# Kernel tuning notes

Measured on AMD Instinct MI355X. Metric: run time of the kernel, lower is better.

## Reference

```python
import jax, jax.numpy as jnp
import numpy as np

EPS = 1e-5

def conv3x3(x, w, b, stride=1):
    y = jax.lax.conv_general_dilated(x, w, (stride, stride), 'SAME',
                                     dimension_numbers=('NCHW', 'OIHW', 'NCHW'))
    return y + b[None, :, None, None]

def batchnorm_train(x, gamma, beta):
    # training-mode BN: batch statistics over (N, H, W)
    mean = x.mean(axis=(0, 2, 3), keepdims=True)
    var = x.var(axis=(0, 2, 3), keepdims=True)
    xh = (x - mean) * jax.lax.rsqrt(var + EPS)
    return xh * gamma[None, :, None, None] + beta[None, :, None, None]

def haar_dwt2(x):
    # pywt.dwt2(x, 'db1') on last two axes; even H,W so 'symmetric' padding is a no-op.
    # a = (x0 + x1)/sqrt2, d = (x0 - x1)/sqrt2 per axis -> 2x2 block combinations / 2.
    x00 = x[:, :, 0::2, 0::2]
    x01 = x[:, :, 0::2, 1::2]
    x10 = x[:, :, 1::2, 0::2]
    x11 = x[:, :, 1::2, 1::2]
    cA = (x00 + x01 + x10 + x11) * 0.5
    cH = (x00 + x01 - x10 - x11) * 0.5  # pywt 'da': detail along rows
    cV = (x00 - x01 + x10 - x11) * 0.5  # pywt 'ad': detail along cols
    cD = (x00 - x01 - x10 + x11) * 0.5
    return cA, cH, cV, cD


def setup_inputs() -> dict:
    key = jax.random.key(0)
    ks = jax.random.split(key, 8)
    N, in_c, out_c, H, W = 4, 3, 64, 512, 512

    def kaiming(k, shape):
        fan_in = shape[1] * shape[2] * shape[3]
        return jax.random.normal(k, shape, jnp.float32) * np.sqrt(2.0 / fan_in)

    inputs = jax.random.normal(ks[0], (N, in_c, H, W), jnp.float32)
    return {
        'inputs': inputs,
        # conv_block: conv1 -> bn1 -> conv2 -> bn2 -> relu
        'w1': kaiming(ks[1], (out_c, in_c, 3, 3)),
        'b1': jnp.zeros((out_c,), jnp.float32),
        'g1': jnp.ones((out_c,), jnp.float32),
        'be1': jnp.zeros((out_c,), jnp.float32),
        'w2': kaiming(ks[2], (out_c, out_c, 3, 3)),
        'b2': jnp.zeros((out_c,), jnp.float32),
        'g2': jnp.ones((out_c,), jnp.float32),
        'be2': jnp.zeros((out_c,), jnp.float32),
        # conv_dwt_block: conv(out_c*4 -> out_c) -> bn -> relu
        'w3': kaiming(ks[3], (out_c, out_c * 4, 3, 3)),
        'b3': jnp.zeros((out_c,), jnp.float32),
        'g3': jnp.ones((out_c,), jnp.float32),
        'be3': jnp.zeros((out_c,), jnp.float32),
    }


def reference(inputs, w1, b1, g1, be1, w2, b2, g2, be2, w3, b3, g3, be3):
    # conv_block
    x = conv3x3(inputs, w1, b1)
    x = batchnorm_train(x, g1, be1)
    x = conv3x3(x, w2, b2)
    x = batchnorm_train(x, g2, be2)
    skip_con = jax.nn.relu(x)

    # original detaches skip_con before the (CPU pywt) DWT -> no grad through this branch
    dwt_in = jax.lax.stop_gradient(skip_con)
    cA, cH, cV, cD = haar_dwt2(dwt_in)
    dwt = jnp.concatenate((cA, cH, cV, cD), axis=1)  # [N, 4*out_c, H/2, W/2]

    y = conv3x3(dwt, w3, b3)
    y = batchnorm_train(y, g3, be3)
    dwt_out = jax.nn.relu(y)
    return dwt_out, skip_con
```

## Files before the change

### kernel.cpp

```cpp
#include <hip/hip_runtime.h>
#include <cstdint>

typedef float f32x4 __attribute__((ext_vector_type(4)));
typedef __bf16 bf16x8 __attribute__((ext_vector_type(8)));
typedef unsigned int uint32;
typedef unsigned short ushort_t;

__device__ __forceinline__ ushort_t f2bf(float f) {
    uint32 u = __builtin_bit_cast(uint32, f);
    u = (u + 0x7fffu + ((u >> 16) & 1u)) >> 16;
    return (ushort_t)u;
}
__device__ __forceinline__ float bf2f(ushort_t h) {
    return __builtin_bit_cast(float, (uint32)h << 16);
}

__global__ __launch_bounds__(256) void im2col1_kernel(
    const float* __restrict__ in,
    ushort_t* __restrict__ P)
{
    int px = blockIdx.x * 256 + threadIdx.x;
    int n = px >> 18, rem = px & 262143;
    int y = rem >> 9, x = rem & 511;
    ushort_t pv[32];
#pragma unroll
    for (int ci = 0; ci < 3; ++ci)
#pragma unroll
        for (int t = 0; t < 9; ++t) {
            int dy = t / 3 - 1, dx = t % 3 - 1;
            int yy = y + dy, xx = x + dx;
            bool v = ((unsigned)yy < 512u) && ((unsigned)xx < 512u);
            pv[ci * 9 + t] = v ? f2bf(in[((n * 3 + ci) * 512 + yy) * 512 + xx])
                               : (ushort_t)0;
        }
#pragma unroll
    for (int k = 27; k < 32; ++k) pv[k] = 0;
    uint4* dst = (uint4*)(P + (size_t)px * 32);
    dst[0] = *(uint4*)(pv);
    dst[1] = *(uint4*)(pv + 8);
    dst[2] = *(uint4*)(pv + 16);
    dst[3] = *(uint4*)(pv + 24);
}

__global__ void prepw1_kernel(const float* __restrict__ w1,
                              ushort_t* __restrict__ Wsw1)
{
    int i = blockIdx.x * 256 + threadIdx.x;
    int ii = i & 7, lane = (i >> 3) & 63, nt = i >> 9;
    int cout = nt * 16 + (lane & 15);
    int k = (lane >> 4) * 8 + ii;
    Wsw1[i] = (k < 27) ? f2bf(w1[cout * 27 + k]) : (ushort_t)0;
}

__global__ __launch_bounds__(256) void gemm1_kernel(
    const ushort_t* __restrict__ P,
    const ushort_t* __restrict__ Wsw1,
    const float* __restrict__ b1,
    ushort_t* __restrict__ X1)
{
    int tid = threadIdx.x;
    int wave = tid >> 6, lane = tid & 63;
    int lp = lane & 15, lg = lane >> 4;
    int pxb = blockIdx.x * 256 + wave * 64;

    bf16x8 wf[4];
#pragma unroll
    for (int nt = 0; nt < 4; ++nt)
        wf[nt] = *(const bf16x8*)(Wsw1 + (nt * 64 + lane) * 8);

    f32x4 acc[4][4];
#pragma unroll
    for (int a = 0; a < 4; ++a)
#pragma unroll
        for (int b = 0; b < 4; ++b) acc[a][b] = (f32x4){0.f, 0.f, 0.f, 0.f};

#pragma unroll
    for (int nf = 0; nf < 4; ++nf) {
        bf16x8 bfrag = *(const bf16x8*)(P + (size_t)(pxb + nf * 16 + lp) * 32 + lg * 8);
#pragma unroll
        for (int nt = 0; nt < 4; ++nt)
            acc[nt][nf] = __builtin_amdgcn_mfma_f32_16x16x32_bf16(
                wf[nt], bfrag, acc[nt][nf], 0, 0, 0);
    }

#pragma unroll
    for (int nf = 0; nf < 4; ++nf) {
        size_t px = (size_t)pxb + nf * 16 + lp;
#pragma unroll
        for (int nt = 0; nt < 4; ++nt) {
            ushort_t ov[4];
#pragma unroll
            for (int r = 0; r < 4; ++r)
                ov[r] = f2bf(acc[nt][nf][r] + b1[nt * 16 + lg * 4 + r]);
            *(ushort4*)(X1 + px * 64 + nt * 16 + lg * 4) = *(ushort4*)ov;
        }
    }
}

__global__ __launch_bounds__(256) void stats_kernel(
    const ushort_t* __restrict__ X, float* __restrict__ sums, int Mpx)
{
    int tid = threadIdx.x;
    int cb = (tid & 7) * 8;
    int pr = tid >> 3;
    float s[8], q[8];
#pragma unroll
    for (int j = 0; j < 8; ++j) { s[j] = 0.f; q[j] = 0.f; }

    for (int p = blockIdx.x * 32 + pr; p < Mpx; p += gridDim.x * 32) {
        uint4 raw = *(const uint4*)(X + (size_t)p * 64 + cb);
        const ushort_t* up = (const ushort_t*)&raw;
#pragma unroll
        for (int j = 0; j < 8; ++j) {
            float f = bf2f(up[j]);
            s[j] += f; q[j] += f * f;
        }
    }
    __shared__ float ls[32][64];
#pragma unroll
    for (int j = 0; j < 8; ++j) ls[pr][cb + j] = s[j];
    __syncthreads();
    float S = 0.f;
    if (tid < 64) for (int r = 0; r < 32; ++r) S += ls[r][tid];
    __syncthreads();
#pragma unroll
    for (int j = 0; j < 8; ++j) ls[pr][cb + j] = q[j];
    __syncthreads();
    if (tid < 64) {
        float Q = 0.f;
        for (int r = 0; r < 32; ++r) Q += ls[r][tid];
        int bkt = (blockIdx.x & 31) * 128;
        atomicAdd(&sums[bkt + tid], S);
        atomicAdd(&sums[bkt + 64 + tid], Q);
    }
}

__global__ void finalize_kernel(const float* __restrict__ stats,
                                const float* __restrict__ gamma,
                                const float* __restrict__ beta,
                                float inv_cnt, float* __restrict__ scsh)
{
    int c = threadIdx.x;
    float S = 0.f, Q = 0.f;
    for (int b = 0; b < 32; ++b) {
        S += stats[b * 128 + c];
        Q += stats[b * 128 + 64 + c];
    }
    float mean = S * inv_cnt;
    float var  = Q * inv_cnt - mean * mean;
    float rs   = rsqrtf(var + 1e-5f);
    float sc   = gamma[c] * rs;
    scsh[c]      = sc;
    scsh[64 + c] = beta[c] - mean * sc;
}

__global__ __launch_bounds__(256) void prepw_kernel(
    const float* __restrict__ w, const float* __restrict__ scale,
    ushort_t* __restrict__ Wsw, int CIN)
{
    int i = blockIdx.x * 256 + threadIdx.x;
    int KC = CIN >> 5;
    int ii = i & 7, lane = (i >> 3) & 63, nt = (i >> 9) & 3;
    int rest = i >> 11;
    int kc = rest % KC, t = rest / KC;
    if (t >= 9) return;
    int cout = nt * 16 + (lane & 15);
    int cin  = kc * 32 + (lane >> 4) * 8 + ii;
    float v = w[(cout * CIN + cin) * 9 + t];
    if (scale) v *= scale[cin];
    Wsw[i] = f2bf(v);
}

__global__ void prepT_kernel(const float* __restrict__ w2,
                             const float* __restrict__ shift,
                             float* __restrict__ T)
{
    int idx = threadIdx.x;
    if (idx < 576) {
        int t = idx / 64, cout = idx % 64;
        float s = 0.f;
        for (int cin = 0; cin < 64; ++cin)
            s += w2[(cout * 64 + cin) * 9 + t] * shift[cin];
        T[idx] = s;
    }
    __syncthreads();
    if (idx < 64) {
        float s = 0.f;
        for (int t = 0; t < 9; ++t) s += T[t * 64 + idx];
        T[576 + idx] = s;
    }
}

template <int CIN, bool HAS_T, int HH, int WW>
__global__ __launch_bounds__(256, 3) void conv_mfma2_kernel(
    const ushort_t* __restrict__ X,
    const ushort_t* __restrict__ Wsw,
    const float* __restrict__ T,
    const float* __restrict__ bias,
    ushort_t* __restrict__ Y,
    float* __restrict__ stats)
{
    constexpr int KC  = CIN >> 5;
    constexpr int NCH = CIN >> 6;
    constexpr int COLS_B = WW >> 6;
    constexpr int ROWS_B = HH >> 2;

    __shared__ ushort_t tile[25344];
    __shared__ float sred[4][128];

    int nwg = gridDim.x;
    int bid = blockIdx.x;
    int cpx = nwg >> 3;
    int bs  = (bid & 7) * cpx + (bid >> 3);

    int tid  = threadIdx.x;
    int wave = tid >> 6, lane = tid & 63;
    int lp = lane & 15, lg = lane >> 4;

    int tmp = bs;
    int ctile = tmp % COLS_B;  tmp /= COLS_B;
    int rtile = tmp % ROWS_B;
    int n     = tmp / ROWS_B;
    int y0 = rtile << 2, x0 = ctile << 6;
    int y  = y0 + wave;

    f32x4 acc[4][4];
#pragma unroll
    for (int a = 0; a < 4; ++a)
#pragma unroll
        for (int b = 0; b < 4; ++b) acc[a][b] = (f32x4){0.f, 0.f, 0.f, 0.f};

#pragma unroll 1
    for (int c = 0; c < NCH; ++c) {
        if (c) __syncthreads();
#pragma unroll 1
        for (int i = tid; i < 3168; i += 256) {
            int lpx = i >> 3, cb = i & 7;
            int ry = lpx / 66, cx = lpx - ry * 66;
            int gy = y0 - 1 + ry, gx = x0 - 1 + cx;
            uint4 v = {0u, 0u, 0u, 0u};
            if (((unsigned)gy < (unsigned)HH) && ((unsigned)gx < (unsigned)WW))
                v = *(const uint4*)(X + ((size_t)(n * HH + gy) * WW + gx) * CIN + c * 64 + cb * 8);
            *(uint4*)((char*)tile + lpx * 128 + ((cb * 16) ^ ((lpx & 7) << 4))) = v;
        }
        __syncthreads();

#pragma unroll
        for (int t = 0; t < 9; ++t) {
            int dy = t / 3 - 1, dx = t % 3 - 1;
            int prow = (wave + 1 + dy) * 66 + (1 + dx) + lp;
#pragma unroll
            for (int kk = 0; kk < 2; ++kk) {
                int kc = c * 2 + kk;
                bf16x8 wf[4];
#pragma unroll
                for (int nt = 0; nt < 4; ++nt)
                    wf[nt] = *(const bf16x8*)(Wsw + (size_t)(((t * KC + kc) << 2) + nt) * 512 + lane * 8);
#pragma unroll
                for (int nf = 0; nf < 4; ++nf) {
                    int lpix = prow + nf * 16;
                    bf16x8 bfrag = *(const bf16x8*)((const char*)tile + lpix * 128
                                       + ((lg * 16 + kk * 64) ^ ((lpix & 7) << 4)));
#pragma unroll
                    for (int nt = 0; nt < 4; ++nt)
                        acc[nt][nf] = __builtin_amdgcn_mfma_f32_16x16x32_bf16(
                            wf[nt], bfrag, acc[nt][nf], 0, 0, 0);
                }
            }
        }
    }

    bool top = (y == 0), bot = (y == HH - 1);
    float s16[16], q16[16];
#pragma unroll
    for (int j = 0; j < 16; ++j) { s16[j] = 0.f; q16[j] = 0.f; }

    size_t rowbase = ((size_t)(n * HH + y) * WW) * 64;
#pragma unroll
    for (int nf = 0; nf < 4; ++nf) {
        int x = x0 + nf * 16 + lp;
        bool lft = (x == 0), rgt = (x == WW - 1);
        bool edge = top | bot | lft | rgt;
#pragma unroll
        for (int nt = 0; nt < 4; ++nt) {
            ushort_t ov[4];
#pragma unroll
            for (int r = 0; r < 4; ++r) {
                int ch = nt * 16 + lg * 4 + r;
                float o = acc[nt][nf][r] + bias[ch];
                if (HAS_T) {
                    o += T[576 + ch];
                    if (edge) {
#pragma unroll
                        for (int t = 0; t < 9; ++t) {
                            int dy = t / 3 - 1, dx = t % 3 - 1;
                            bool miss = (top && dy < 0) || (bot && dy > 0) ||
                                        (lft && dx < 0) || (rgt && dx > 0);
                            if (miss) o -= T[t * 64 + ch];
                        }
                    }
                }
                s16[nt * 4 + r] += o;
                q16[nt * 4 + r] += o * o;
                ov[r] = f2bf(o);
            }
            *(ushort4*)(Y + rowbase + (size_t)x * 64 + nt * 16 + lg * 4) = *(ushort4*)ov;
        }
    }

#pragma unroll
    for (int off = 1; off < 16; off <<= 1)
#pragma unroll
        for (int j = 0; j < 16; ++j) {
            s16[j] += __shfl_xor(s16[j], off);
            q16[j] += __shfl_xor(q16[j], off);
        }
    if (lp == 0) {
#pragma unroll
        for (int nt = 0; nt < 4; ++nt)
#pragma unroll
            for (int r = 0; r < 4; ++r) {
                int ch = nt * 16 + lg * 4 + r;
                sred[wave][ch]      = s16[nt * 4 + r];
                sred[wave][64 + ch] = q16[nt * 4 + r];
            }
    }
    __syncthreads();
    if (tid < 128) {
        float tot = sred[0][tid] + sred[1][tid] + sred[2][tid] + sred[3][tid];
        atomicAdd(&stats[(bs & 31) * 128 + tid], tot);
    }
}

__global__ __launch_bounds__(256) void bn2_dwt_skip_kernel(
    const ushort_t* __restrict__ X2, const float* __restrict__ scsh,
    float* __restrict__ skip,
    ushort_t* __restrict__ X3)
{
    __shared__ float v[128][65];
    int tid = threadIdx.x;
    int b = blockIdx.x;
    int n  = b >> 11;
    int r2 = b & 2047;
    int y0 = (r2 >> 3) << 1;
    int x0 = (r2 & 7) << 6;

#pragma unroll
    for (int k = 0; k < 4; ++k) {
        int q  = tid + k * 256;
        int px = q >> 3;
        int cb = (q & 7) * 8;
        int gy = y0 + (px >> 6);
        int gx = x0 + (px & 63);
        uint4 raw = *(const uint4*)(X2 + ((size_t)(n * 512 + gy) * 512 + gx) * 64 + cb);
        const ushort_t* up = (const ushort_t*)&raw;
#pragma unroll
        for (int j = 0; j < 8; ++j) {
            float f = bf2f(up[j]);
            float o = f * scsh[cb + j] + scsh[64 + cb + j];
            v[px][cb + j] = fmaxf(o, 0.f);
        }
    }
    __syncthreads();

    {
        int c = tid >> 2, sub = tid & 3;
#pragma unroll
        for (int rr = 0; rr < 2; ++rr) {
            float* orow = skip + ((size_t)(n * 64 + c) * 512 + (y0 + rr)) * 512 + x0;
#pragma unroll
            for (int qq = 0; qq < 4; ++qq) {
                int xb = qq * 16 + sub * 4;
                float4 w4;
                w4.x = v[rr * 64 + xb + 0][c];
                w4.y = v[rr * 64 + xb + 1][c];
                w4.z = v[rr * 64 + xb + 2][c];
                w4.w = v[rr * 64 + xb + 3][c];
                *(float4*)(orow + xb) = w4;
            }
        }
    }
    {
        int c = tid & 63, jj = tid >> 6;
        int yq = y0 >> 1, xq = x0 >> 1;
#pragma unroll
        for (int it = 0; it < 8; ++it) {
            int xl = jj * 8 + it;
            float x00 = v[2 * xl][c],      x01 = v[2 * xl + 1][c];
            float x10 = v[64 + 2 * xl][c], x11 = v[64 + 2 * xl + 1][c];
            float cA = (x00 + x01 + x10 + x11) * 0.5f;
            float cH = (x00 + x01 - x10 - x11) * 0.5f;
            float cV = (x00 - x01 + x10 - x11) * 0.5f;
            float cD = (x00 - x01 - x10 + x11) * 0.5f;
            ushort_t* dst = X3 + ((size_t)(n * 256 + yq) * 256 + xq + xl) * 256 + c;
            dst[0]   = f2bf(cA);
            dst[64]  = f2bf(cH);
            dst[128] = f2bf(cV);
            dst[192] = f2bf(cD);
        }
    }
}

__global__ __launch_bounds__(256) void bn3_kernel(
    const ushort_t* __restrict__ X4, const float* __restrict__ scsh,
    float* __restrict__ out)
{
    __shared__ float v[64][65];
    int tid = threadIdx.x;
    int b = blockIdx.x;
    int n  = b >> 10;
    int r2 = b & 1023;
    int y  = r2 >> 2;
    int x0 = (r2 & 3) << 6;

#pragma unroll
    for (int k = 0; k < 2; ++k) {
        int q  = tid + k * 256;
        int px = q >> 3;
        int cb = (q & 7) * 8;
        uint4 raw = *(const uint4*)(X4 + ((size_t)(n * 256 + y) * 256 + x0 + px) * 64 + cb);
        const ushort_t* up = (const ushort_t*)&raw;
#pragma unroll
        for (int j = 0; j < 8; ++j) {
            float f = bf2f(up[j]);
            float o = f * scsh[cb + j] + scsh[64 + cb + j];
            v[px][cb + j] = fmaxf(o, 0.f);
        }
    }
    __syncthreads();
    int c = tid >> 2, sub = tid & 3;
    float* orow = out + ((size_t)(n * 64 + c) * 256 + y) * 256 + x0;
#pragma unroll
    for (int qq = 0; qq < 4; ++qq) {
        int xb = qq * 16 + sub * 4;
        float4 w4;
        w4.x = v[xb + 0][c];
        w4.y = v[xb + 1][c];
        w4.z = v[xb + 2][c];
        w4.w = v[xb + 3][c];
        *(float4*)(orow + xb) = w4;
    }
}

extern "C" void kernel_launch(void* const* d_in, const int* in_sizes, int n_in,
                              void* d_out, int out_size, void* d_ws, size_t ws_size,
                              hipStream_t stream)
{
    const float* in  = (const float*)d_in[0];
    const float* w1  = (const float*)d_in[1];
    const float* b1  = (const float*)d_in[2];
    const float* g1  = (const float*)d_in[3];
    const float* be1 = (const float*)d_in[4];
    const float* w2  = (const float*)d_in[5];
    const float* b2  = (const float*)d_in[6];
    const float* g2  = (const float*)d_in[7];
    const float* be2 = (const float*)d_in[8];
    const float* w3  = (const float*)d_in[9];
    const float* b3  = (const float*)d_in[10];
    const float* g3  = (const float*)d_in[11];
    const float* be3 = (const float*)d_in[12];

    float* out     = (float*)d_out;
    float* dwt_out = out;
    float* skip    = out + 16777216;

    char* ws = (char*)d_ws;
    ushort_t* X1 = (ushort_t*)ws;
    ushort_t* X2 = (ushort_t*)(ws + 134217728);
    ushort_t* P  = X2;
    ushort_t* X3 = X1;
    ushort_t* X4 = X2;
    char* aux = ws + 268435456;
    float* stats1 = (float*)(aux);
    float* stats2 = (float*)(aux + 16384);
    float* stats3 = (float*)(aux + 32768);
    float* scsh1  = (float*)(aux + 49152);
    float* scsh2  = (float*)(aux + 49664);
    float* scsh3  = (float*)(aux + 50176);
    float* T2     = (float*)(aux + 50688);
    ushort_t* Wsw2 = (ushort_t*)(aux + 57344);
    ushort_t* Wsw3 = (ushort_t*)(aux + 131072);
    ushort_t* Wsw1 = (ushort_t*)(aux + 425984);

    hipMemsetAsync(aux, 0, 49152, stream);

    im2col1_kernel<<<4096, 256, 0, stream>>>(in, P);
    prepw1_kernel<<<8, 256, 0, stream>>>(w1, Wsw1);
    gemm1_kernel<<<4096, 256, 0, stream>>>(P, Wsw1, b1, X1);
    stats_kernel<<<512, 256, 0, stream>>>(X1, stats1, 1048576);
    finalize_kernel<<<1, 64, 0, stream>>>(stats1, g1, be1, 1.f / 1048576.f, scsh1);
    prepw_kernel<<<144, 256, 0, stream>>>(w2, scsh1, Wsw2, 64);
    prepT_kernel<<<1, 576, 0, stream>>>(w2, scsh1 + 64, T2);

    conv_mfma2_kernel<64, true, 512, 512><<<4096, 256, 0, stream>>>(
        X1, Wsw2, T2, b2, X2, stats2);
    finalize_kernel<<<1, 64, 0, stream>>>(stats2, g2, be2, 1.f / 1048576.f, scsh2);

    bn2_dwt_skip_kernel<<<8192, 256, 0, stream>>>(X2, scsh2, skip, X3);

    prepw_kernel<<<576, 256, 0, stream>>>(w3, nullptr, Wsw3, 256);
    conv_mfma2_kernel<256, false, 256, 256><<<1024, 256, 0, stream>>>(
        X3, Wsw3, nullptr, b3, X4, stats3);
    finalize_kernel<<<1, 64, 0, stream>>>(stats3, g3, be3, 1.f / 262144.f, scsh3);

    bn3_kernel<<<4096, 256, 0, stream>>>(X4, scsh3, dwt_out);
}
```

Measured before the change: 614.1 us.

## Fuse BN1 stats into gemm1 and double-buffer conv LDS staging across tiles

```diff
diff --git a/kernel.cpp b/kernel.cpp
--- a/kernel.cpp
+++ b/kernel.cpp
@@ -56,8 +56,10 @@
     const ushort_t* __restrict__ P,
     const ushort_t* __restrict__ Wsw1,
     const float* __restrict__ b1,
-    ushort_t* __restrict__ X1)
-{
+    ushort_t* __restrict__ X1,
+    float* __restrict__ stats)
+{
+    __shared__ float sred[4][128];
     int tid = threadIdx.x;
     int wave = tid >> 6, lane = tid & 63;
     int lp = lane & 15, lg = lane >> 4;
@@ -83,6 +85,10 @@
                 wf[nt], bfrag, acc[nt][nf], 0, 0, 0);
     }
 
+    float s16[16], q16[16];
+#pragma unroll
+    for (int j = 0; j < 16; ++j) { s16[j] = 0.f; q16[j] = 0.f; }
+
 #pragma unroll
     for (int nf = 0; nf < 4; ++nf) {
         size_t px = (size_t)pxb + nf * 16 + lp;
@@ -90,48 +96,37 @@
         for (int nt = 0; nt < 4; ++nt) {
             ushort_t ov[4];
 #pragma unroll
-            for (int r = 0; r < 4; ++r)
-                ov[r] = f2bf(acc[nt][nf][r] + b1[nt * 16 + lg * 4 + r]);
+            for (int r = 0; r < 4; ++r) {
+                float o = acc[nt][nf][r] + b1[nt * 16 + lg * 4 + r];
+                s16[nt * 4 + r] += o;
+                q16[nt * 4 + r] += o * o;
+                ov[r] = f2bf(o);
+            }
             *(ushort4*)(X1 + px * 64 + nt * 16 + lg * 4) = *(ushort4*)ov;
         }
     }
-}
-
-__global__ __launch_bounds__(256) void stats_kernel(
-    const ushort_t* __restrict__ X, float* __restrict__ sums, int Mpx)
-{
-    int tid = threadIdx.x;
-    int cb = (tid & 7) * 8;
-    int pr = tid >> 3;
-    float s[8], q[8];
-#pragma unroll
-    for (int j = 0; j < 8; ++j) { s[j] = 0.f; q[j] = 0.f; }
-
-    for (int p = blockIdx.x * 32 + pr; p < Mpx; p += gridDim.x * 32) {
-        uint4 raw = *(const uint4*)(X + (size_t)p * 64 + cb);
-        const ushort_t* up = (const ushort_t*)&raw;
-#pragma unroll
-        for (int j = 0; j < 8; ++j) {
-            float f = bf2f(up[j]);
-            s[j] += f; q[j] += f * f;
-        }
-    }
-    __shared__ float ls[32][64];
-#pragma unroll
-    for (int j = 0; j < 8; ++j) ls[pr][cb + j] = s[j];
+
+#pragma unroll
+    for (int off = 1; off < 16; off <<= 1)
+#pragma unroll
+        for (int j = 0; j < 16; ++j) {
+            s16[j] += __shfl_xor(s16[j], off);
+            q16[j] += __shfl_xor(q16[j], off);
+        }
+    if (lp == 0) {
+#pragma unroll
+        for (int nt = 0; nt < 4; ++nt)
+#pragma unroll
+            for (int r = 0; r < 4; ++r) {
+                int ch = nt * 16 + lg * 4 + r;
+                sred[wave][ch]      = s16[nt * 4 + r];
+                sred[wave][64 + ch] = q16[nt * 4 + r];
+            }
+    }
     __syncthreads();
-    float S = 0.f;
-    if (tid < 64) for (int r = 0; r < 32; ++r) S += ls[r][tid];
-    __syncthreads();
-#pragma unroll
-    for (int j = 0; j < 8; ++j) ls[pr][cb + j] = q[j];
-    __syncthreads();
-    if (tid < 64) {
-        float Q = 0.f;
-        for (int r = 0; r < 32; ++r) Q += ls[r][tid];
-        int bkt = (blockIdx.x & 31) * 128;
-        atomicAdd(&sums[bkt + tid], S);
-        atomicAdd(&sums[bkt + 64 + tid], Q);
+    if (tid < 128) {
+        float tot = sred[0][tid] + sred[1][tid] + sred[2][tid] + sred[3][tid];
+        atomicAdd(&stats[(blockIdx.x & 31) * 128 + tid], tot);
     }
 }
 
@@ -191,8 +186,8 @@
     }
 }
 
-template <int CIN, bool HAS_T, int HH, int WW>
-__global__ __launch_bounds__(256, 3) void conv_mfma2_kernel(
+template <int CIN, bool HAS_T, int HH, int WW, int TILES>
+__global__ __launch_bounds__(256, 3) void conv_mfma3_kernel(
     const ushort_t* __restrict__ X,
     const ushort_t* __restrict__ Wsw,
     const float* __restrict__ T,
@@ -200,12 +195,14 @@
     ushort_t* __restrict__ Y,
     float* __restrict__ stats)
 {
-    constexpr int KC  = CIN >> 5;
-    constexpr int NCH = CIN >> 6;
-    constexpr int COLS_B = WW >> 6;
-    constexpr int ROWS_B = HH >> 2;
-
-    __shared__ ushort_t tile[25344];
+    constexpr int KC     = CIN >> 5;
+    constexpr int STAGES = TILES * KC;
+    constexpr int CSTR   = WW / (64 * TILES);
+    constexpr int RSTR   = HH >> 2;
+    constexpr int NLD    = 1584;
+
+    __shared__ ushort_t lds0[12672];
+    __shared__ ushort_t lds1[12672];
     __shared__ float sred[4][128];
 
     int nwg = gridDim.x;
@@ -218,114 +215,143 @@
     int lp = lane & 15, lg = lane >> 4;
 
     int tmp = bs;
-    int ctile = tmp % COLS_B;  tmp /= COLS_B;
-    int rtile = tmp % ROWS_B;
-    int n     = tmp / ROWS_B;
-    int y0 = rtile << 2, x0 = ctile << 6;
+    int cs = tmp % CSTR;  tmp /= CSTR;
+    int rs = tmp % RSTR;
+    int n  = tmp / RSTR;
+    int y0 = rs << 2, x0 = cs * (64 * TILES);
     int y  = y0 + wave;
 
+    for (int i = tid; i < 512; i += 256) ((float*)sred)[i] = 0.f;
+
     f32x4 acc[4][4];
 #pragma unroll
     for (int a = 0; a < 4; ++a)
 #pragma unroll
         for (int b = 0; b < 4; ++b) acc[a][b] = (f32x4){0.f, 0.f, 0.f, 0.f};
 
+    uint4 rbuf[7];
+
+    auto issue_stage = [&](int s) {
+        int tj = s / KC, c = s - tj * KC;
+        int xt = x0 + tj * 64;
+#pragma unroll
+        for (int j = 0; j < 7; ++j) {
+            int idx = tid + j * 256;
+            uint4 v = {0u, 0u, 0u, 0u};
+            if (idx < NLD) {
+                int p  = idx >> 2;
+                int ry = p / 66, cx = p - ry * 66;
+                int gy = y0 - 1 + ry, gx = xt - 1 + cx;
+                if (((unsigned)gy < (unsigned)HH) && ((unsigned)gx < (unsigned)WW))
+                    v = *(const uint4*)(X + ((size_t)(n * HH + gy) * WW + gx) * CIN
+                                          + c * 32 + (idx & 3) * 8);
+            }
+            rbuf[j] = v;
+        }
+    };
+    auto write_stage = [&](ushort_t* buf) {
+#pragma unroll
+        for (int j = 0; j < 7; ++j) {
+            int idx = tid + j * 256;
+            if (idx < NLD) ((uint4*)buf)[idx] = rbuf[j];
+        }
+    };
+
+    issue_stage(0);
+    write_stage(lds0);
+    __syncthreads();
+
+    ushort_t* cur = lds0;
+    ushort_t* nxt = lds1;
+
 #pragma unroll 1
-    for (int c = 0; c < NCH; ++c) {
-        if (c) __syncthreads();
-#pragma unroll 1
-        for (int i = tid; i < 3168; i += 256) {
-            int lpx = i >> 3, cb = i & 7;
-            int ry = lpx / 66, cx = lpx - ry * 66;
-            int gy = y0 - 1 + ry, gx = x0 - 1 + cx;
-            uint4 v = {0u, 0u, 0u, 0u};
-            if (((unsigned)gy < (unsigned)HH) && ((unsigned)gx < (unsigned)WW))
-                v = *(const uint4*)(X + ((size_t)(n * HH + gy) * WW + gx) * CIN + c * 64 + cb * 8);
-            *(uint4*)((char*)tile + lpx * 128 + ((cb * 16) ^ ((lpx & 7) << 4))) = v;
-        }
+    for (int s = 0; s < STAGES; ++s) {
+        int tj = s / KC, c = s - tj * KC;
+        if (s + 1 < STAGES) issue_stage(s + 1);
+
+#pragma unroll
+        for (int t = 0; t < 9; ++t) {
+            const int dy = t / 3 - 1, dx = t % 3 - 1;
+            bf16x8 wf[4];
+#pragma unroll
+            for (int nt = 0; nt < 4; ++nt)
+                wf[nt] = *(const bf16x8*)(Wsw + (size_t)(((t * KC + c) << 2) + nt) * 512 + lane * 8);
+            int prow = (wave + 1 + dy) * 66 + (1 + dx) + lp;
+#pragma unroll
+            for (int nf = 0; nf < 4; ++nf) {
+                int px = prow + nf * 16;
+                bf16x8 bfrag = *(const bf16x8*)((const char*)cur + px * 64 + lg * 16);
+#pragma unroll
+                for (int nt = 0; nt < 4; ++nt)
+                    acc[nt][nf] = __builtin_amdgcn_mfma_f32_16x16x32_bf16(
+                        wf[nt], bfrag, acc[nt][nf], 0, 0, 0);
+            }
+        }
+
+        if (c == KC - 1) {
+            int xt = x0 + tj * 64;
+            bool top = (y == 0), bot = (y == HH - 1);
+            float s16[16], q16[16];
+            size_t rowbase = ((size_t)(n * HH + y) * WW) * 64;
+#pragma unroll
+            for (int nf = 0; nf < 4; ++nf) {
+                int x = xt + nf * 16 + lp;
+                bool lft = (x == 0), rgt = (x == WW - 1);
+                bool edge = top | bot | lft | rgt;
+#pragma unroll
+                for (int nt = 0; nt < 4; ++nt) {
+                    ushort_t ov[4];
+#pragma unroll
+                    for (int r = 0; r < 4; ++r) {
+                        int ch = nt * 16 + lg * 4 + r;
+                        float o = acc[nt][nf][r] + bias[ch];
+                        if (HAS_T) {
+                            o += T[576 + ch];
+                            if (edge) {
+#pragma unroll
+                                for (int t = 0; t < 9; ++t) {
+                                    int dy = t / 3 - 1, dx = t % 3 - 1;
+                                    bool miss = (top && dy < 0) || (bot && dy > 0) ||
+                                                (lft && dx < 0) || (rgt && dx > 0);
+                                    if (miss) o -= T[t * 64 + ch];
+                                }
+                            }
+                        }
+                        if (nf == 0) { s16[nt * 4 + r] = o; q16[nt * 4 + r] = o * o; }
+                        else         { s16[nt * 4 + r] += o; q16[nt * 4 + r] += o * o; }
+                        ov[r] = f2bf(o);
+                    }
+                    *(ushort4*)(Y + rowbase + (size_t)x * 64 + nt * 16 + lg * 4) = *(ushort4*)ov;
+                }
+            }
+#pragma unroll
+            for (int off = 1; off < 16; off <<= 1)
+#pragma unroll
+                for (int j = 0; j < 16; ++j) {
+                    s16[j] += __shfl_xor(s16[j], off);
+                    q16[j] += __shfl_xor(q16[j], off);
+                }
+            if (lp == 0) {
+#pragma unroll
+                for (int nt = 0; nt < 4; ++nt)
+#pragma unroll
+                    for (int r = 0; r < 4; ++r) {
+                        int ch = nt * 16 + lg * 4 + r;
+                        sred[wave][ch]      += s16[nt * 4 + r];
+                        sred[wave][64 + ch] += q16[nt * 4 + r];
+                    }
+            }
+#pragma unroll
+            for (int a = 0; a < 4; ++a)
+#pragma unroll
+                for (int b = 0; b < 4; ++b) acc[a][b] = (f32x4){0.f, 0.f, 0.f, 0.f};
+        }
+
+        if (s + 1 < STAGES) write_stage(nxt);
         __syncthreads();
-
-#pragma unroll
-        for (int t = 0; t < 9; ++t) {
-            int dy = t / 3 - 1, dx = t % 3 - 1;
-            int prow = (wave + 1 + dy) * 66 + (1 + dx) + lp;
-#pragma unroll
-            for (int kk = 0; kk < 2; ++kk) {
-                int kc = c * 2 + kk;
-                bf16x8 wf[4];
-#pragma unroll
-                for (int nt = 0; nt < 4; ++nt)
-                    wf[nt] = *(const bf16x8*)(Wsw + (size_t)(((t * KC + kc) << 2) + nt) * 512 + lane * 8);
-#pragma unroll
-                for (int nf = 0; nf < 4; ++nf) {
-                    int lpix = prow + nf * 16;
-                    bf16x8 bfrag = *(const bf16x8*)((const char*)tile + lpix * 128
-                                       + ((lg * 16 + kk * 64) ^ ((lpix & 7) << 4)));
-#pragma unroll
-                    for (int nt = 0; nt < 4; ++nt)
-                        acc[nt][nf] = __builtin_amdgcn_mfma_f32_16x16x32_bf16(
-                            wf[nt], bfrag, acc[nt][nf], 0, 0, 0);
-                }
-            }
-        }
-    }
-
-    bool top = (y == 0), bot = (y == HH - 1);
-    float s16[16], q16[16];
-#pragma unroll
-    for (int j = 0; j < 16; ++j) { s16[j] = 0.f; q16[j] = 0.f; }
-
-    size_t rowbase = ((size_t)(n * HH + y) * WW) * 64;
-#pragma unroll
-    for (int nf = 0; nf < 4; ++nf) {
-        int x = x0 + nf * 16 + lp;
-        bool lft = (x == 0), rgt = (x == WW - 1);
-        bool edge = top | bot | lft | rgt;
-#pragma unroll
-        for (int nt = 0; nt < 4; ++nt) {
-            ushort_t ov[4];
-#pragma unroll
-            for (int r = 0; r < 4; ++r) {
-                int ch = nt * 16 + lg * 4 + r;
-                float o = acc[nt][nf][r] + bias[ch];
-                if (HAS_T) {
-                    o += T[576 + ch];
-                    if (edge) {
-#pragma unroll
-                        for (int t = 0; t < 9; ++t) {
-                            int dy = t / 3 - 1, dx = t % 3 - 1;
-                            bool miss = (top && dy < 0) || (bot && dy > 0) ||
-                                        (lft && dx < 0) || (rgt && dx > 0);
-                            if (miss) o -= T[t * 64 + ch];
-                        }
-                    }
-                }
-                s16[nt * 4 + r] += o;
-                q16[nt * 4 + r] += o * o;
-                ov[r] = f2bf(o);
-            }
-            *(ushort4*)(Y + rowbase + (size_t)x * 64 + nt * 16 + lg * 4) = *(ushort4*)ov;
-        }
-    }
-
-#pragma unroll
-    for (int off = 1; off < 16; off <<= 1)
-#pragma unroll
-        for (int j = 0; j < 16; ++j) {
-            s16[j] += __shfl_xor(s16[j], off);
-            q16[j] += __shfl_xor(q16[j], off);
-        }
-    if (lp == 0) {
-#pragma unroll
-        for (int nt = 0; nt < 4; ++nt)
-#pragma unroll
-            for (int r = 0; r < 4; ++r) {
-                int ch = nt * 16 + lg * 4 + r;
-                sred[wave][ch]      = s16[nt * 4 + r];
-                sred[wave][64 + ch] = q16[nt * 4 + r];
-            }
-    }
-    __syncthreads();
+        ushort_t* t2 = cur; cur = nxt; nxt = t2;
+    }
+
     if (tid < 128) {
         float tot = sred[0][tid] + sred[1][tid] + sred[2][tid] + sred[3][tid];
         atomicAdd(&stats[(bs & 31) * 128 + tid], tot);
@@ -486,20 +512,19 @@
 
     im2col1_kernel<<<4096, 256, 0, stream>>>(in, P);
     prepw1_kernel<<<8, 256, 0, stream>>>(w1, Wsw1);
-    gemm1_kernel<<<4096, 256, 0, stream>>>(P, Wsw1, b1, X1);
-    stats_kernel<<<512, 256, 0, stream>>>(X1, stats1, 1048576);
+    gemm1_kernel<<<4096, 256, 0, stream>>>(P, Wsw1, b1, X1, stats1);
     finalize_kernel<<<1, 64, 0, stream>>>(stats1, g1, be1, 1.f / 1048576.f, scsh1);
     prepw_kernel<<<144, 256, 0, stream>>>(w2, scsh1, Wsw2, 64);
     prepT_kernel<<<1, 576, 0, stream>>>(w2, scsh1 + 64, T2);
 
-    conv_mfma2_kernel<64, true, 512, 512><<<4096, 256, 0, stream>>>(
+    conv_mfma3_kernel<64, true, 512, 512, 4><<<1024, 256, 0, stream>>>(
         X1, Wsw2, T2, b2, X2, stats2);
     finalize_kernel<<<1, 64, 0, stream>>>(stats2, g2, be2, 1.f / 1048576.f, scsh2);
 
     bn2_dwt_skip_kernel<<<8192, 256, 0, stream>>>(X2, scsh2, skip, X3);
 
     prepw_kernel<<<576, 256, 0, stream>>>(w3, nullptr, Wsw3, 256);
-    conv_mfma2_kernel<256, false, 256, 256><<<1024, 256, 0, stream>>>(
+    conv_mfma3_kernel<256, false, 256, 256, 1><<<1024, 256, 0, stream>>>(
         X3, Wsw3, nullptr, b3, X4, stats3);
     finalize_kernel<<<1, 64, 0, stream>>>(stats3, g3, be3, 1.f / 262144.f, scsh3);
 
```

Result: no change. 620.5 us (+1.0%).
